# Kernel tuning notes

Hardware: AMD Instinct MI355X
Metric: run time of the kernel (lower is better)

The kernel has to match this reference:

```python
import jax, jax.numpy as jnp
import numpy as np

N_NODES = 100000
N_REL = 8
IN_DIM = 64
HID = 128
OUT = 64
N_EDGES = 640000


def setup_inputs() -> dict:
    key = jax.random.key(0)
    ks = jax.random.split(key, 24)

    def w(k, shape, fan_in):
        return jax.random.normal(k, shape, jnp.float32) / np.sqrt(fan_in).astype(np.float32)

    inp = {}
    inp["emb"] = jax.random.normal(ks[0], (N_NODES, IN_DIM), jnp.float32)
    dims = [(IN_DIM, HID), (HID, HID), (HID, HID // 2), (HID // 2, OUT)]
    for i, (di, do) in enumerate(dims, 1):
        inp[f"W{i}"] = w(ks[3 * i], (N_REL, di, do), di)      # per-relation weight
        inp[f"R{i}"] = w(ks[3 * i + 1], (di, do), di)          # root weight
        inp[f"B{i}"] = jnp.zeros((do,), jnp.float32)           # bias
    inp["g1"] = jnp.ones((HID,), jnp.float32)
    inp["b1"] = jnp.zeros((HID,), jnp.float32)
    inp["g2"] = jnp.ones((HID,), jnp.float32)
    inp["b2"] = jnp.zeros((HID,), jnp.float32)
    inp["ei"] = jax.random.randint(ks[20], (2, N_EDGES), 0, N_NODES, jnp.int32)
    inp["et"] = jax.random.randint(ks[21], (N_EDGES,), 0, N_REL, jnp.int32)
    return inp


def rgcn(x, ei, et, W, Wr, b):
    # PyG RGCNConv (aggr='mean'): out_i = x_i @ Wroot + b + sum_r mean_{j in N_r(i)} x_j @ W_r
    # Aggregate-then-transform: mean x[src] per (dst, rel) bin, then per-relation GEMM.
    n, r, d = x.shape[0], W.shape[0], x.shape[1]
    src, dst = ei[0], ei[1]
    seg = dst * r + et                                   # combined (node, relation) segment id
    agg = jax.ops.segment_sum(x[src], seg, num_segments=n * r)          # [N*R, d]
    cnt = jax.ops.segment_sum(jnp.ones((src.shape[0],), x.dtype), seg, num_segments=n * r)
    agg = (agg / jnp.maximum(cnt, 1.0)[:, None]).reshape(n, r, d)       # mean per relation
    return jnp.einsum('nri,rio->no', agg, W) + x @ Wr + b


def layer_norm(x, g, b, eps=1e-5):
    mu = jnp.mean(x, axis=-1, keepdims=True)
    var = jnp.mean((x - mu) ** 2, axis=-1, keepdims=True)
    return (x - mu) * jax.lax.rsqrt(var + eps) * g + b


def reference(emb, W1, R1, B1, W2, R2, B2, W3, R3, B3, W4, R4, B4, g1, b1, g2, b2, ei, et):
    # dropout is eval-mode identity
    x = jax.nn.relu(rgcn(emb, ei, et, W1, R1, B1))
    x = layer_norm(x, g1, b1)
    identity = x
    x = jax.nn.relu(rgcn(x, ei, et, W2, R2, B2))
    x = layer_norm(x + identity, g2, b2)
    x = jax.nn.relu(rgcn(x, ei, et, W3, R3, B3))
    return rgcn(x, ei, et, W4, R4, B4)
```

## Files before the change

### kernel.cpp

```cpp
#include <hip/hip_runtime.h>
#include <math.h>

#define NN 100000
#define NR 8
#define NE 640000
#define SEGN (NN * NR)
#define SPB 2048
#define NSB ((SEGN + SPB - 1) / SPB)

#define TILES 1563
#define HT1 782
#define HT2 781
#define HP1 (HT1 * 64)
#define HP2 (HT2 * 64)
#define HPF (TILES * 64)

typedef __attribute__((ext_vector_type(8))) __bf16 bf16x8;
typedef __attribute__((ext_vector_type(4))) float  f32x4;

__device__ __forceinline__ float bf2f(unsigned short b) {
    return __uint_as_float((unsigned)b << 16);
}
__device__ __forceinline__ unsigned short f2bf(float v) {
    __bf16 b = (__bf16)v;
    return __builtin_bit_cast(unsigned short, b);
}


__global__ __launch_bounds__(256) void count_kernel(
    const int* __restrict__ dst, const int* __restrict__ et, unsigned* __restrict__ cnt) {
    int e = blockIdx.x * 256 + threadIdx.x;
    if (e < NE) atomicAdd(&cnt[(size_t)et[e] * NN + dst[e]], 1u);
}

__global__ __launch_bounds__(256) void scan1_kernel(
    const unsigned* __restrict__ cnt, unsigned* __restrict__ bsum) {
    __shared__ unsigned red[256];
    int b = blockIdx.x, t = threadIdx.x;
    int i0 = b * SPB;
    unsigned s = 0;
#pragma unroll
    for (int k = 0; k < SPB / 256; ++k) {
        int i = i0 + k * 256 + t;
        if (i < SEGN) s += cnt[i];
    }
    red[t] = s;
    __syncthreads();
    for (int off = 128; off >= 1; off >>= 1) {
        if (t < off) red[t] += red[t + off];
        __syncthreads();
    }
    if (t == 0) bsum[b] = red[0];
}

__global__ __launch_bounds__(512) void scan2_kernel(
    unsigned* __restrict__ bsum, int* __restrict__ segoff) {
    __shared__ unsigned buf[512];
    int t = threadIdx.x;
    unsigned v = (t < NSB) ? bsum[t] : 0u;
    buf[t] = v;
    __syncthreads();
    for (int off = 1; off < 512; off <<= 1) {
        unsigned w = (t >= off) ? buf[t - off] : 0u;
        __syncthreads();
        buf[t] += w;
        __syncthreads();
    }
    if (t < NSB) bsum[t] = buf[t] - v;
    if (t == 0) segoff[SEGN] = NE;
}

__global__ __launch_bounds__(256) void scan3_kernel(
    const unsigned* __restrict__ cnt, const unsigned* __restrict__ bsum,
    int* __restrict__ segoff) {
    __shared__ unsigned lc[SPB];
    __shared__ unsigned tsum[256];
    int b = blockIdx.x, t = threadIdx.x;
    int i0 = b * SPB;
#pragma unroll
    for (int k = 0; k < SPB / 256; ++k) {
        int i = i0 + k * 256 + t;
        lc[k * 256 + t] = (i < SEGN) ? cnt[i] : 0u;
    }
    __syncthreads();
    unsigned s = 0;
#pragma unroll
    for (int k = 0; k < 8; ++k) s += lc[t * 8 + k];
    tsum[t] = s;
    __syncthreads();
    for (int off = 1; off < 256; off <<= 1) {
        unsigned w = (t >= off) ? tsum[t - off] : 0u;
        __syncthreads();
        tsum[t] += w;
        __syncthreads();
    }
    unsigned base = bsum[b] + tsum[t] - s;
#pragma unroll
    for (int k = 0; k < 8; ++k) {
        unsigned c = lc[t * 8 + k];
        lc[t * 8 + k] = base;
        base += c;
    }
    __syncthreads();
#pragma unroll
    for (int k = 0; k < SPB / 256; ++k) {
        int i = i0 + k * 256 + t;
        if (i < SEGN) segoff[i] = (int)lc[k * 256 + t];
    }
}

__global__ __launch_bounds__(256) void fill_kernel(
    const int* __restrict__ src, const int* __restrict__ dst, const int* __restrict__ et,
    const int* __restrict__ segoff, unsigned* __restrict__ cursor, int* __restrict__ esrc) {
    int e = blockIdx.x * 256 + threadIdx.x;
    if (e >= NE) return;
    int d = dst[e];
    int seg = et[e] * NN + d;
    int pos = segoff[seg] + (int)atomicAdd(&cursor[seg], 1u);
    esrc[pos] = src[e] | ((d & 3) << 17);
}

__global__ __launch_bounds__(256) void conv_emb(
    const float* __restrict__ emb, ushort* __restrict__ embb) {
    int i = blockIdx.x * 256 + threadIdx.x;
    if (i * 4 >= NN * 64) return;
    f32x4 v = *(const f32x4*)(emb + (size_t)i * 4);
    ushort4 o;
    o.x = f2bf(v[0]); o.y = f2bf(v[1]); o.z = f2bf(v[2]); o.w = f2bf(v[3]);
    *(ushort4*)(embb + (size_t)i * 4) = o;
}


template <int D, int O>
__global__ __launch_bounds__(256) void pack_kernel(
    const float* __restrict__ W, const float* __restrict__ Wr, __bf16* __restrict__ Wp) {
    constexpr int KT = D / 32, NTN = O / 16;
    int idx = blockIdx.x * 256 + threadIdx.x;
    if (idx >= (NR + 1) * KT * NTN * 64) return;
    int l = idx & 63;
    int rest = idx >> 6;
    int nt = rest % NTN; rest /= NTN;
    int kt = rest % KT;
    int r  = rest / KT;
    const float* srcw = (r < NR) ? (W + (size_t)r * D * O) : Wr;
    int n  = nt * 16 + (l & 15);
    int k0 = kt * 32 + (l >> 4) * 8;
    bf16x8 v;
#pragma unroll
    for (int j = 0; j < 8; ++j) {
        int p  = k0 + j;
        int kd = (D == 128) ? ((p >> 1) + ((p & 1) << 6)) : p;
        v[j] = (__bf16)srcw[(size_t)kd * O + n];
    }
    *(bf16x8*)(Wp + (size_t)idx * 8) = v;
}


template <int D, int XF>
__global__ __launch_bounds__(256) void gather_kernel(
    const void* __restrict__ xin, const int* __restrict__ segoff,
    const int* __restrict__ esrc, ushort* __restrict__ agg,
    int nbase, int agg_off, int HP)
{
    int wv = threadIdx.x >> 6, ln = threadIdx.x & 63;
    int r  = blockIdx.y;
    int i0 = blockIdx.x * 16 + wv * 4;
    int n0 = nbase + i0;

    const ushort*   xb = (const ushort*)xin;
    const unsigned* xs = (const unsigned*)xin;

    float ax[4] = {0, 0, 0, 0}, ay[4] = {0, 0, 0, 0};
    int eo[5];
#pragma unroll
    for (int k = 0; k <= 4; ++k) {
        int node = n0 + k; if (node > NN) node = NN;
        eo[k] = segoff[r * NN + node];
    }
    for (int ei = eo[0]; ei < eo[4]; ei += 4) {
        int nb = eo[4] - ei; if (nb > 4) nb = 4;
        int mm[4]; float vx[4], vy[4];
#pragma unroll
        for (int b = 0; b < 4; ++b) mm[b] = (b < nb) ? esrc[ei + b] : 0;
#pragma unroll
        for (int b = 0; b < 4; ++b) {
            if (b < nb) {
                int s = mm[b] & 0x1FFFF;
                if constexpr (XF == 1) {
                    unsigned w = xs[(size_t)s * 64 + ln];
                    vx[b] = bf2f((unsigned short)(w & 0xFFFFu));
                    vy[b] = bf2f((unsigned short)(w >> 16));
                } else {
                    vx[b] = bf2f(xb[(size_t)s * 64 + ln]);
                }
            }
        }
#pragma unroll
        for (int b = 0; b < 4; ++b) {
            if (b < nb) {
                int k = mm[b] >> 17;
#pragma unroll
                for (int kk = 0; kk < 4; ++kk) {
                    ax[kk] += (kk == k) ? vx[b] : 0.0f;
                    if constexpr (D == 128) ay[kk] += (kk == k) ? vy[b] : 0.0f;
                }
            }
        }
    }
#pragma unroll
    for (int k = 0; k < 4; ++k) {
        int c = eo[k + 1] - eo[k];
        float sc = (c > 0) ? 1.0f / (float)c : 0.0f;
        size_t row = ((size_t)r * HP + agg_off + i0 + k) * D;
        if constexpr (D == 128) {
            unsigned st = (unsigned)f2bf(ax[k] * sc) | ((unsigned)f2bf(ay[k] * sc) << 16);
            *((unsigned*)(agg + row) + ln) = st;
        } else {
            agg[row + ln] = f2bf(ax[k] * sc);
        }
    }
}


template <int D, int O, int MODE, int XF, int OF>
__global__ __launch_bounds__(64, (D == 64) ? 4 : 3) void gemm_layer(
    const ushort* __restrict__ agg, const __bf16* __restrict__ Wp,
    const float* __restrict__ bias, const float* __restrict__ gamma,
    const float* __restrict__ beta, const unsigned* __restrict__ xres,
    const void* __restrict__ xroot, void* __restrict__ outv, int base, int HP)
{
    constexpr int KT = D / 32, NTN = O / 16;
    constexpr int PD = (D == 64) ? 8 : 4;
    int ln = threadIdx.x, lg = ln >> 4, lm = ln & 15;
    int i0 = blockIdx.x * 16;

    const ushort* abase = agg + ((size_t)(i0 + lm)) * D + lg * 8;

    bf16x8 Aring[PD][KT];
#pragma unroll
    for (int r = 0; r < PD; ++r) {
        const ushort* ar = abase + (size_t)r * HP * D;
#pragma unroll
        for (int kt = 0; kt < KT; ++kt)
            Aring[r][kt] = *(const bf16x8*)(ar + kt * 32);
    }

    bf16x8 Aroot[KT];
    {
        int nrow = base + i0 + lm;
        if (nrow >= NN) nrow = NN - 1;
#pragma unroll
        for (int kt = 0; kt < KT; ++kt) {
            if constexpr (XF == 1) {
                Aroot[kt] = *(const bf16x8*)((const ushort*)xroot +
                                             (size_t)nrow * 128 + kt * 32 + lg * 8);
            } else {
                Aroot[kt] = *(const bf16x8*)((const ushort*)xroot +
                                             (size_t)nrow * 64 + kt * 32 + lg * 8);
            }
        }
    }

    f32x4 acc[NTN];
#pragma unroll
    for (int nt = 0; nt < NTN; ++nt)
#pragma unroll
        for (int q = 0; q < 4; ++q) acc[nt][q] = 0.0f;

#pragma unroll
    for (int r = 0; r < NR; ++r) {
        const __bf16* bp = Wp + (((size_t)(r * KT) * NTN) << 9) + (ln << 3);
#pragma unroll
        for (int kt = 0; kt < KT; ++kt) {
            const __bf16* bpk = bp + (((size_t)(kt * NTN)) << 9);
#pragma unroll
            for (int nt = 0; nt < NTN; ++nt) {
                bf16x8 B = *(const bf16x8*)(bpk + ((size_t)nt << 9));
                acc[nt] = __builtin_amdgcn_mfma_f32_16x16x32_bf16(
                    Aring[r % PD][kt], B, acc[nt], 0, 0, 0);
            }
        }
        if (r + PD < NR) {
            const ushort* an = abase + (size_t)(r + PD) * HP * D;
#pragma unroll
            for (int kt = 0; kt < KT; ++kt)
                Aring[(r + PD) % PD][kt] = *(const bf16x8*)(an + kt * 32);
        }
    }
    {
        const __bf16* bp = Wp + (((size_t)(8 * KT) * NTN) << 9) + (ln << 3);
#pragma unroll
        for (int kt = 0; kt < KT; ++kt) {
            const __bf16* bpk = bp + (((size_t)(kt * NTN)) << 9);
#pragma unroll
            for (int nt = 0; nt < NTN; ++nt) {
                bf16x8 B = *(const bf16x8*)(bpk + ((size_t)nt << 9));
                acc[nt] = __builtin_amdgcn_mfma_f32_16x16x32_bf16(Aroot[kt], B, acc[nt], 0, 0, 0);
            }
        }
    }

    float bb[NTN], gg[NTN], be[NTN];
#pragma unroll
    for (int nt = 0; nt < NTN; ++nt) {
        bb[nt] = bias[nt * 16 + lm];
        if constexpr (MODE <= 1) {
            gg[nt] = gamma[nt * 16 + lm];
            be[nt] = beta[nt * 16 + lm];
        } else {
            gg[nt] = 0.0f; be[nt] = 0.0f;
        }
    }
#pragma unroll
    for (int q = 0; q < 4; ++q) {
        int row = lg * 4 + q;
        int n = base + i0 + row;
        int nc = (n < NN) ? n : 0;
        float v[NTN];
#pragma unroll
        for (int nt = 0; nt < NTN; ++nt) {
            v[nt] = acc[nt][q] + bb[nt];
            if constexpr (MODE <= 2) v[nt] = fmaxf(v[nt], 0.0f);
            if constexpr (MODE == 1) {
                unsigned w = xres[(size_t)nc * 64 + (nt & 3) * 16 + lm];
                v[nt] += bf2f((unsigned short)((nt < 4) ? (w & 0xFFFFu) : (w >> 16)));
            }
        }
        if constexpr (MODE <= 1) {
            float s1 = 0.0f, s2 = 0.0f;
#pragma unroll
            for (int nt = 0; nt < NTN; ++nt) { s1 += v[nt]; s2 += v[nt] * v[nt]; }
#pragma unroll
            for (int off = 1; off < 16; off <<= 1) {
                s1 += __shfl_xor(s1, off, 64);
                s2 += __shfl_xor(s2, off, 64);
            }
            float mu  = s1 * (1.0f / O);
            float var = s2 * (1.0f / O) - mu * mu;
            float rs  = rsqrtf(var + 1e-5f);
#pragma unroll
            for (int nt = 0; nt < NTN; ++nt) v[nt] = (v[nt] - mu) * rs * gg[nt] + be[nt];
        }
        if (n < NN) {
            if constexpr (OF == 0) {
#pragma unroll
                for (int nt = 0; nt < NTN; ++nt)
                    __builtin_nontemporal_store(
                        v[nt], (float*)outv + (size_t)n * O + nt * 16 + lm);
            } else if constexpr (OF == 1) {
#pragma unroll
                for (int nt = 0; nt < 4; ++nt)
                    ((unsigned*)outv)[(size_t)n * 64 + nt * 16 + lm] =
                        (unsigned)f2bf(v[nt]) | ((unsigned)f2bf(v[nt + 4]) << 16);
            } else {
#pragma unroll
                for (int nt = 0; nt < NTN; ++nt)
                    ((ushort*)outv)[(size_t)n * 64 + nt * 16 + lm] = f2bf(v[nt]);
            }
        }
    }
}


extern "C" void kernel_launch(void* const* d_in, const int* in_sizes, int n_in,
                              void* d_out, int out_size, void* d_ws, size_t ws_size,
                              hipStream_t stream) {
    const float* emb = (const float*)d_in[0];
    const float* W1  = (const float*)d_in[1];
    const float* R1  = (const float*)d_in[2];
    const float* B1  = (const float*)d_in[3];
    const float* W2  = (const float*)d_in[4];
    const float* R2  = (const float*)d_in[5];
    const float* B2  = (const float*)d_in[6];
    const float* W3  = (const float*)d_in[7];
    const float* R3  = (const float*)d_in[8];
    const float* B3  = (const float*)d_in[9];
    const float* W4  = (const float*)d_in[10];
    const float* R4  = (const float*)d_in[11];
    const float* B4  = (const float*)d_in[12];
    const float* g1  = (const float*)d_in[13];
    const float* b1  = (const float*)d_in[14];
    const float* g2  = (const float*)d_in[15];
    const float* b2  = (const float*)d_in[16];
    const int*   ei  = (const int*)d_in[17];
    const int*   et  = (const int*)d_in[18];
    const int* srcp = ei;
    const int* dstp = ei + NE;

    char* ws = (char*)d_ws;
    if (ws_size < 185721872u) return;
    int*      segoff = (int*)(ws + 0);
    int*      esrc   = (int*)(ws + 3200016);
    __bf16*   Wp1    = (__bf16*)(ws + 5760016);
    __bf16*   Wp2    = (__bf16*)(ws + 5907472);
    __bf16*   Wp3    = (__bf16*)(ws + 6202384);
    __bf16*   Wp4    = (__bf16*)(ws + 6349840);
    ushort*   embb   = (ushort*)(ws + 6423568);
    void*     x1     = (void*)(ws + 19223568);
    void*     x2     = (void*)(ws + 44823568);
    void*     x3     = (void*)(ws + 70423568);
    ushort*   agg    = (ushort*)(ws + 83223568);
    unsigned* cnt    = (unsigned*)(ws + 83223568);
    unsigned* cursor = (unsigned*)(ws + 86423568);
    unsigned* bsum   = (unsigned*)(ws + 89623568);
    float*    outp   = (float*)d_out;

    hipMemsetAsync(cnt, 0, 3200000, stream);
    hipMemsetAsync(cursor, 0, 3200000, stream);

    count_kernel<<<(NE + 255) / 256, 256, 0, stream>>>(dstp, et, cnt);
    scan1_kernel<<<NSB, 256, 0, stream>>>(cnt, bsum);
    scan2_kernel<<<1, 512, 0, stream>>>(bsum, segoff);
    scan3_kernel<<<NSB, 256, 0, stream>>>(cnt, bsum, segoff);
    fill_kernel<<<(NE + 255) / 256, 256, 0, stream>>>(
        srcp, dstp, et, segoff, cursor, esrc);
    conv_emb<<<(NN * 64 / 4 + 255) / 256, 256, 0, stream>>>(emb, embb);

    pack_kernel<64, 128><<<(9 * 2 * 8 * 64 + 255) / 256, 256, 0, stream>>>(W1, R1, Wp1);
    pack_kernel<128, 128><<<(9 * 4 * 8 * 64 + 255) / 256, 256, 0, stream>>>(W2, R2, Wp2);
    pack_kernel<128, 64><<<(9 * 4 * 4 * 64 + 255) / 256, 256, 0, stream>>>(W3, R3, Wp3);
    pack_kernel<64, 64><<<(9 * 2 * 4 * 64 + 255) / 256, 256, 0, stream>>>(W4, R4, Wp4);

    gather_kernel<64, 2><<<dim3(HP1 / 16, 8), 256, 0, stream>>>(embb, segoff, esrc, agg, 0, 0, HPF);
    gather_kernel<64, 2><<<dim3(HP2 / 16, 8), 256, 0, stream>>>(embb, segoff, esrc, agg, HP1, HP1, HPF);
    gemm_layer<64, 128, 0, 2, 1><<<HPF / 16, 64, 0, stream>>>(
        agg, Wp1, B1, g1, b1, nullptr, embb, x1, 0, HPF);

    gather_kernel<128, 1><<<dim3(25024 / 16, 8), 256, 0, stream>>>(x1, segoff, esrc, agg, 0, 0, HP1);
    gather_kernel<128, 1><<<dim3(25024 / 16, 8), 256, 0, stream>>>(x1, segoff, esrc, agg, 25024, 25024, HP1);
    gemm_layer<128, 128, 1, 1, 1><<<HP1 / 16, 64, 0, stream>>>(
        agg, Wp2, B2, g2, b2, (const unsigned*)x1, x1, x2, 0, HP1);
    gather_kernel<128, 1><<<dim3(25024 / 16, 8), 256, 0, stream>>>(x1, segoff, esrc, agg, HP1, 0, HP2);
    gather_kernel<128, 1><<<dim3(24960 / 16, 8), 256, 0, stream>>>(x1, segoff, esrc, agg, HP1 + 25024, 25024, HP2);
    gemm_layer<128, 128, 1, 1, 1><<<HP2 / 16, 64, 0, stream>>>(
        agg, Wp2, B2, g2, b2, (const unsigned*)x1, x1, x2, HP1, HP2);

    gather_kernel<128, 1><<<dim3(25024 / 16, 8), 256, 0, stream>>>(x2, segoff, esrc, agg, 0, 0, HP1);
    gather_kernel<128, 1><<<dim3(25024 / 16, 8), 256, 0, stream>>>(x2, segoff, esrc, agg, 25024, 25024, HP1);
    gemm_layer<128, 64, 2, 1, 2><<<HP1 / 16, 64, 0, stream>>>(
        agg, Wp3, B3, nullptr, nullptr, nullptr, x2, x3, 0, HP1);
    gather_kernel<128, 1><<<dim3(25024 / 16, 8), 256, 0, stream>>>(x2, segoff, esrc, agg, HP1, 0, HP2);
    gather_kernel<128, 1><<<dim3(24960 / 16, 8), 256, 0, stream>>>(x2, segoff, esrc, agg, HP1 + 25024, 25024, HP2);
    gemm_layer<128, 64, 2, 1, 2><<<HP2 / 16, 64, 0, stream>>>(
        agg, Wp3, B3, nullptr, nullptr, nullptr, x2, x3, HP1, HP2);

    gather_kernel<64, 2><<<dim3(HP1 / 16, 8), 256, 0, stream>>>(x3, segoff, esrc, agg, 0, 0, HPF);
    gather_kernel<64, 2><<<dim3(HP2 / 16, 8), 256, 0, stream>>>(x3, segoff, esrc, agg, HP1, HP1, HPF);
    gemm_layer<64, 64, 3, 2, 0><<<HPF / 16, 64, 0, stream>>>(
        agg, Wp4, B4, nullptr, nullptr, nullptr, x3, outp, 0, HPF);
}
```

Before: 714.0 us.

## Compute two 16-row M tiles per wave so each weight fragment is reused

Each single-wave GEMM block now handles 32 node rows as two 16-row MFMA tiles. Every loaded weight fragment feeds both tiles, which halves weight-load traffic per output row and halves the grid size. The per-relation A-fragment prefetch ring and the occupancy hint in launch_bounds are removed, and A is loaded per relation just before use. The risk is more exposed load latency, plus higher register pressure from doubled accumulators, which may reduce occupancy.

```diff
diff --git a/kernel.cpp b/kernel.cpp
--- a/kernel.cpp
+++ b/kernel.cpp
@@ -223,79 +223,72 @@
 
 
 template <int D, int O, int MODE, int XF, int OF>
-__global__ __launch_bounds__(64, (D == 64) ? 4 : 3) void gemm_layer(
+__global__ __launch_bounds__(64) void gemm_layer(
     const ushort* __restrict__ agg, const __bf16* __restrict__ Wp,
     const float* __restrict__ bias, const float* __restrict__ gamma,
     const float* __restrict__ beta, const unsigned* __restrict__ xres,
     const void* __restrict__ xroot, void* __restrict__ outv, int base, int HP)
 {
     constexpr int KT = D / 32, NTN = O / 16;
-    constexpr int PD = (D == 64) ? 8 : 4;
     int ln = threadIdx.x, lg = ln >> 4, lm = ln & 15;
-    int i0 = blockIdx.x * 16;
-
-    const ushort* abase = agg + ((size_t)(i0 + lm)) * D + lg * 8;
-
-    bf16x8 Aring[PD][KT];
-#pragma unroll
-    for (int r = 0; r < PD; ++r) {
-        const ushort* ar = abase + (size_t)r * HP * D;
-#pragma unroll
-        for (int kt = 0; kt < KT; ++kt)
-            Aring[r][kt] = *(const bf16x8*)(ar + kt * 32);
-    }
-
-    bf16x8 Aroot[KT];
+    int i0 = blockIdx.x * 32;
+
+    const ushort* abase0 = agg + ((size_t)(i0 + lm)) * D + lg * 8;
+    const ushort* abase1 = agg + ((size_t)(i0 + 16 + lm)) * D + lg * 8;
+
+    f32x4 acc[2][NTN];
+#pragma unroll
+    for (int m = 0; m < 2; ++m)
+#pragma unroll
+        for (int nt = 0; nt < NTN; ++nt)
+#pragma unroll
+            for (int q = 0; q < 4; ++q) acc[m][nt][q] = 0.0f;
+
+#pragma unroll
+    for (int r = 0; r < NR; ++r) {
+        bf16x8 A0[KT], A1[KT];
+        const ushort* ar0 = abase0 + (size_t)r * HP * D;
+        const ushort* ar1 = abase1 + (size_t)r * HP * D;
+#pragma unroll
+        for (int kt = 0; kt < KT; ++kt) {
+            A0[kt] = *(const bf16x8*)(ar0 + kt * 32);
+            A1[kt] = *(const bf16x8*)(ar1 + kt * 32);
+        }
+        const __bf16* bp = Wp + (((size_t)(r * KT) * NTN) << 9) + (ln << 3);
+#pragma unroll
+        for (int kt = 0; kt < KT; ++kt) {
+            const __bf16* bpk = bp + (((size_t)(kt * NTN)) << 9);
+#pragma unroll
+            for (int nt = 0; nt < NTN; ++nt) {
+                bf16x8 B = *(const bf16x8*)(bpk + ((size_t)nt << 9));
+                acc[0][nt] = __builtin_amdgcn_mfma_f32_16x16x32_bf16(A0[kt], B, acc[0][nt], 0, 0, 0);
+                acc[1][nt] = __builtin_amdgcn_mfma_f32_16x16x32_bf16(A1[kt], B, acc[1][nt], 0, 0, 0);
+            }
+        }
+    }
     {
-        int nrow = base + i0 + lm;
-        if (nrow >= NN) nrow = NN - 1;
+        bf16x8 A0[KT], A1[KT];
+        int nr0 = base + i0 + lm;       if (nr0 >= NN) nr0 = NN - 1;
+        int nr1 = base + i0 + 16 + lm;  if (nr1 >= NN) nr1 = NN - 1;
 #pragma unroll
         for (int kt = 0; kt < KT; ++kt) {
             if constexpr (XF == 1) {
-                Aroot[kt] = *(const bf16x8*)((const ushort*)xroot +
-                                             (size_t)nrow * 128 + kt * 32 + lg * 8);
+                A0[kt] = *(const bf16x8*)((const ushort*)xroot + (size_t)nr0 * 128 + kt * 32 + lg * 8);
+                A1[kt] = *(const bf16x8*)((const ushort*)xroot + (size_t)nr1 * 128 + kt * 32 + lg * 8);
             } else {
-                Aroot[kt] = *(const bf16x8*)((const ushort*)xroot +
-                                             (size_t)nrow * 64 + kt * 32 + lg * 8);
-            }
-        }
-    }
-
-    f32x4 acc[NTN];
-#pragma unroll
-    for (int nt = 0; nt < NTN; ++nt)
-#pragma unroll
-        for (int q = 0; q < 4; ++q) acc[nt][q] = 0.0f;
-
-#pragma unroll
-    for (int r = 0; r < NR; ++r) {
-        const __bf16* bp = Wp + (((size_t)(r * KT) * NTN) << 9) + (ln << 3);
+                A0[kt] = *(const bf16x8*)((const ushort*)xroot + (size_t)nr0 * 64 + kt * 32 + lg * 8);
+                A1[kt] = *(const bf16x8*)((const ushort*)xroot + (size_t)nr1 * 64 + kt * 32 + lg * 8);
+            }
+        }
+        const __bf16* bp = Wp + (((size_t)(8 * KT) * NTN) << 9) + (ln << 3);
 #pragma unroll
         for (int kt = 0; kt < KT; ++kt) {
             const __bf16* bpk = bp + (((size_t)(kt * NTN)) << 9);
 #pragma unroll
             for (int nt = 0; nt < NTN; ++nt) {
                 bf16x8 B = *(const bf16x8*)(bpk + ((size_t)nt << 9));
-                acc[nt] = __builtin_amdgcn_mfma_f32_16x16x32_bf16(
-                    Aring[r % PD][kt], B, acc[nt], 0, 0, 0);
-            }
-        }
-        if (r + PD < NR) {
-            const ushort* an = abase + (size_t)(r + PD) * HP * D;
-#pragma unroll
-            for (int kt = 0; kt < KT; ++kt)
-                Aring[(r + PD) % PD][kt] = *(const bf16x8*)(an + kt * 32);
-        }
-    }
-    {
-        const __bf16* bp = Wp + (((size_t)(8 * KT) * NTN) << 9) + (ln << 3);
-#pragma unroll
-        for (int kt = 0; kt < KT; ++kt) {
-            const __bf16* bpk = bp + (((size_t)(kt * NTN)) << 9);
-#pragma unroll
-            for (int nt = 0; nt < NTN; ++nt) {
-                bf16x8 B = *(const bf16x8*)(bpk + ((size_t)nt << 9));
-                acc[nt] = __builtin_amdgcn_mfma_f32_16x16x32_bf16(Aroot[kt], B, acc[nt], 0, 0, 0);
+                acc[0][nt] = __builtin_amdgcn_mfma_f32_16x16x32_bf16(A0[kt], B, acc[0][nt], 0, 0, 0);
+                acc[1][nt] = __builtin_amdgcn_mfma_f32_16x16x32_bf16(A1[kt], B, acc[1][nt], 0, 0, 0);
             }
         }
     }
@@ -312,50 +305,53 @@
         }
     }
 #pragma unroll
-    for (int q = 0; q < 4; ++q) {
-        int row = lg * 4 + q;
-        int n = base + i0 + row;
-        int nc = (n < NN) ? n : 0;
-        float v[NTN];
-#pragma unroll
-        for (int nt = 0; nt < NTN; ++nt) {
-            v[nt] = acc[nt][q] + bb[nt];
-            if constexpr (MODE <= 2) v[nt] = fmaxf(v[nt], 0.0f);
-            if constexpr (MODE == 1) {
-                unsigned w = xres[(size_t)nc * 64 + (nt & 3) * 16 + lm];
-                v[nt] += bf2f((unsigned short)((nt < 4) ? (w & 0xFFFFu) : (w >> 16)));
-            }
-        }
-        if constexpr (MODE <= 1) {
-            float s1 = 0.0f, s2 = 0.0f;
-#pragma unroll
-            for (int nt = 0; nt < NTN; ++nt) { s1 += v[nt]; s2 += v[nt] * v[nt]; }
-#pragma unroll
-            for (int off = 1; off < 16; off <<= 1) {
-                s1 += __shfl_xor(s1, off, 64);
-                s2 += __shfl_xor(s2, off, 64);
-            }
-            float mu  = s1 * (1.0f / O);
-            float var = s2 * (1.0f / O) - mu * mu;
-            float rs  = rsqrtf(var + 1e-5f);
-#pragma unroll
-            for (int nt = 0; nt < NTN; ++nt) v[nt] = (v[nt] - mu) * rs * gg[nt] + be[nt];
-        }
-        if (n < NN) {
-            if constexpr (OF == 0) {
-#pragma unroll
-                for (int nt = 0; nt < NTN; ++nt)
-                    __builtin_nontemporal_store(
-                        v[nt], (float*)outv + (size_t)n * O + nt * 16 + lm);
-            } else if constexpr (OF == 1) {
-#pragma unroll
-                for (int nt = 0; nt < 4; ++nt)
-                    ((unsigned*)outv)[(size_t)n * 64 + nt * 16 + lm] =
-                        (unsigned)f2bf(v[nt]) | ((unsigned)f2bf(v[nt + 4]) << 16);
-            } else {
-#pragma unroll
-                for (int nt = 0; nt < NTN; ++nt)
-                    ((ushort*)outv)[(size_t)n * 64 + nt * 16 + lm] = f2bf(v[nt]);
+    for (int m = 0; m < 2; ++m) {
+#pragma unroll
+        for (int q = 0; q < 4; ++q) {
+            int row = m * 16 + lg * 4 + q;
+            int n = base + i0 + row;
+            int nc = (n < NN) ? n : 0;
+            float v[NTN];
+#pragma unroll
+            for (int nt = 0; nt < NTN; ++nt) {
+                v[nt] = acc[m][nt][q] + bb[nt];
+                if constexpr (MODE <= 2) v[nt] = fmaxf(v[nt], 0.0f);
+                if constexpr (MODE == 1) {
+                    unsigned w = xres[(size_t)nc * 64 + (nt & 3) * 16 + lm];
+                    v[nt] += bf2f((unsigned short)((nt < 4) ? (w & 0xFFFFu) : (w >> 16)));
+                }
+            }
+            if constexpr (MODE <= 1) {
+                float s1 = 0.0f, s2 = 0.0f;
+#pragma unroll
+                for (int nt = 0; nt < NTN; ++nt) { s1 += v[nt]; s2 += v[nt] * v[nt]; }
+#pragma unroll
+                for (int off = 1; off < 16; off <<= 1) {
+                    s1 += __shfl_xor(s1, off, 64);
+                    s2 += __shfl_xor(s2, off, 64);
+                }
+                float mu  = s1 * (1.0f / O);
+                float var = s2 * (1.0f / O) - mu * mu;
+                float rs  = rsqrtf(var + 1e-5f);
+#pragma unroll
+                for (int nt = 0; nt < NTN; ++nt) v[nt] = (v[nt] - mu) * rs * gg[nt] + be[nt];
+            }
+            if (n < NN) {
+                if constexpr (OF == 0) {
+#pragma unroll
+                    for (int nt = 0; nt < NTN; ++nt)
+                        __builtin_nontemporal_store(
+                            v[nt], (float*)outv + (size_t)n * O + nt * 16 + lm);
+                } else if constexpr (OF == 1) {
+#pragma unroll
+                    for (int nt = 0; nt < 4; ++nt)
+                        ((unsigned*)outv)[(size_t)n * 64 + nt * 16 + lm] =
+                            (unsigned)f2bf(v[nt]) | ((unsigned)f2bf(v[nt + 4]) << 16);
+                } else {
+#pragma unroll
+                    for (int nt = 0; nt < NTN; ++nt)
+                        ((ushort*)outv)[(size_t)n * 64 + nt * 16 + lm] = f2bf(v[nt]);
+                }
             }
         }
     }
@@ -423,29 +419,29 @@
 
     gather_kernel<64, 2><<<dim3(HP1 / 16, 8), 256, 0, stream>>>(embb, segoff, esrc, agg, 0, 0, HPF);
     gather_kernel<64, 2><<<dim3(HP2 / 16, 8), 256, 0, stream>>>(embb, segoff, esrc, agg, HP1, HP1, HPF);
-    gemm_layer<64, 128, 0, 2, 1><<<HPF / 16, 64, 0, stream>>>(
+    gemm_layer<64, 128, 0, 2, 1><<<HPF / 32, 64, 0, stream>>>(
         agg, Wp1, B1, g1, b1, nullptr, embb, x1, 0, HPF);
 
     gather_kernel<128, 1><<<dim3(25024 / 16, 8), 256, 0, stream>>>(x1, segoff, esrc, agg, 0, 0, HP1);
     gather_kernel<128, 1><<<dim3(25024 / 16, 8), 256, 0, stream>>>(x1, segoff, esrc, agg, 25024, 25024, HP1);
-    gemm_layer<128, 128, 1, 1, 1><<<HP1 / 16, 64, 0, stream>>>(
+    gemm_layer<128, 128, 1, 1, 1><<<HP1 / 32, 64, 0, stream>>>(
         agg, Wp2, B2, g2, b2, (const unsigned*)x1, x1, x2, 0, HP1);
     gather_kernel<128, 1><<<dim3(25024 / 16, 8), 256, 0, stream>>>(x1, segoff, esrc, agg, HP1, 0, HP2);
     gather_kernel<128, 1><<<dim3(24960 / 16, 8), 256, 0, stream>>>(x1, segoff, esrc, agg, HP1 + 25024, 25024, HP2);
-    gemm_layer<128, 128, 1, 1, 1><<<HP2 / 16, 64, 0, stream>>>(
+    gemm_layer<128, 128, 1, 1, 1><<<HP2 / 32, 64, 0, stream>>>(
         agg, Wp2, B2, g2, b2, (const unsigned*)x1, x1, x2, HP1, HP2);
 
     gather_kernel<128, 1><<<dim3(25024 / 16, 8), 256, 0, stream>>>(x2, segoff, esrc, agg, 0, 0, HP1);
     gather_kernel<128, 1><<<dim3(25024 / 16, 8), 256, 0, stream>>>(x2, segoff, esrc, agg, 25024, 25024, HP1);
-    gemm_layer<128, 64, 2, 1, 2><<<HP1 / 16, 64, 0, stream>>>(
+    gemm_layer<128, 64, 2, 1, 2><<<HP1 / 32, 64, 0, stream>>>(
         agg, Wp3, B3, nullptr, nullptr, nullptr, x2, x3, 0, HP1);
     gather_kernel<128, 1><<<dim3(25024 / 16, 8), 256, 0, stream>>>(x2, segoff, esrc, agg, HP1, 0, HP2);
     gather_kernel<128, 1><<<dim3(24960 / 16, 8), 256, 0, stream>>>(x2, segoff, esrc, agg, HP1 + 25024, 25024, HP2);
-    gemm_layer<128, 64, 2, 1, 2><<<HP2 / 16, 64, 0, stream>>>(
+    gemm_layer<128, 64, 2, 1, 2><<<HP2 / 32, 64, 0, stream>>>(
         agg, Wp3, B3, nullptr, nullptr, nullptr, x2, x3, HP1, HP2);
 
     gather_kernel<64, 2><<<dim3(HP1 / 16, 8), 256, 0, stream>>>(x3, segoff, esrc, agg, 0, 0, HPF);
     gather_kernel<64, 2><<<dim3(HP2 / 16, 8), 256, 0, stream>>>(x3, segoff, esrc, agg, HP1, HP1, HPF);
-    gemm_layer<64, 64, 3, 2, 0><<<HPF / 16, 64, 0, stream>>>(
+    gemm_layer<64, 64, 3, 2, 0><<<HPF / 32, 64, 0, stream>>>(
         agg, Wp4, B4, nullptr, nullptr, nullptr, x3, outp, 0, HPF);
 }
```

Measured after the change: 730.8 us. 2.4% more time.
